# Kernel tuning notes

Measured on AMD Instinct MI355X. Metric: run time of the kernel, lower is better.

Reference implementation:

```python
import jax, jax.numpy as jnp
import numpy as np

D = 128      # feature dim
H = 8        # heads
DH = D // H  # dim per head
N = 100000   # nodes
E = 600000   # edges
BN_EPS = 1e-5


def _bn(x, g, b, m, v):
    # BatchNorm1d in eval mode (running stats)
    return (x - m) * jax.lax.rsqrt(v + BN_EPS) * g + b


def setup_inputs() -> dict:
    key = jax.random.key(0)
    ks = jax.random.split(key, 32)
    s = 1.0 / np.sqrt(D)
    inp = {
        "x": jax.random.normal(ks[0], (N, D), jnp.float32),
        "edge_index": jax.random.randint(ks[1], (2, E), 0, N, jnp.int64),
        # type embeddings (1 node type, 1 edge type)
        "nt_emb": jax.random.normal(ks[2], (1, D), jnp.float32),
        "et_emb": jax.random.normal(ks[3], (1, D), jnp.float32),
        # merge_node_edge_attr: Linear(2D,D) -> BN -> ReLU -> Linear(D,D)
        "mW1": jax.random.normal(ks[4], (2 * D, D), jnp.float32) * s,
        "mb1": jnp.zeros((D,), jnp.float32),
        "m_g": jnp.ones((D,), jnp.float32),
        "m_b": jnp.zeros((D,), jnp.float32),
        "m_m": jax.random.normal(ks[5], (D,), jnp.float32) * 0.1,
        "m_v": jax.random.uniform(ks[6], (D,), jnp.float32, 0.5, 1.5),
        "mW2": jax.random.normal(ks[7], (D, D), jnp.float32) * s,
        "mb2": jnp.zeros((D,), jnp.float32),
        # residual projection (no bias)
        "resW": jax.random.normal(ks[8], (D, D), jnp.float32) * s,
        # attention projections
        "qW": jax.random.normal(ks[9], (D, D), jnp.float32) * s,
        "qb": jnp.zeros((D,), jnp.float32),
        "kW": jax.random.normal(ks[10], (D, D), jnp.float32) * s,
        "kb": jnp.zeros((D,), jnp.float32),
        "vW": jax.random.normal(ks[11], (D, D), jnp.float32) * s,
        "vb": jnp.zeros((D,), jnp.float32),
        # output mlp: Linear -> BN -> LeakyReLU -> Linear
        "oW1": jax.random.normal(ks[12], (D, D), jnp.float32) * s,
        "ob1": jnp.zeros((D,), jnp.float32),
        "o_g": jnp.ones((D,), jnp.float32),
        "o_b": jnp.zeros((D,), jnp.float32),
        "o_m": jax.random.normal(ks[13], (D,), jnp.float32) * 0.1,
        "o_v": jax.random.uniform(ks[14], (D,), jnp.float32, 0.5, 1.5),
        "oW2": jax.random.normal(ks[15], (D, D), jnp.float32) * s,
        "ob2": jnp.zeros((D,), jnp.float32),
    }
    return inp


def reference(x, edge_index, nt_emb, et_emb, mW1, mb1, m_g, m_b, m_m, m_v, mW2, mb2,
              resW, qW, qb, kW, kb, vW, vb, oW1, ob1, o_g, o_b, o_m, o_v, oW2, ob2):
    src = edge_index[0]
    dst = edge_index[1]
    n_nodes = x.shape[0]
    e = edge_index.shape[1]

    # GraphNodeEdgeAttr: edge attrs are constant per edge type; with one node
    # type, edge_attr[0] == edge_attr[1] == merge(cat[node_emb, edge_emb]).
    merged = jnp.concatenate([nt_emb[0], et_emb[0]])          # [2D]
    h = jax.nn.relu(_bn(merged @ mW1 + mb1, m_g, m_b, m_m, m_v))
    ea = h @ mW2 + mb2                                        # [D], broadcasts per edge

    # edge_update: per-edge multi-head attention scores
    x_j = x[src]                                              # [E, D] source feats
    x_i = x[dst]                                              # [E, D] target feats
    q = ((x_j + ea) @ qW + qb).reshape(e, H, DH) / jnp.sqrt(jnp.float32(DH))
    k = ((x_i + ea) @ kW + kb).reshape(e, H, DH)
    msg = (x_j @ vW + vb).reshape(e, H, DH)
    scores = jnp.sum(q * k, axis=2)                           # [E, H]

    # segment softmax keyed by source node index
    smax = jax.ops.segment_max(scores, src, num_segments=n_nodes)
    ex = jnp.exp(scores - smax[src])
    ssum = jax.ops.segment_sum(ex, src, num_segments=n_nodes)
    alpha = ex / ssum[src]                                    # [E, H]

    # message + scatter-add aggregation to destination nodes
    weighted = (msg * alpha[:, :, None]).reshape(e, H * DH)   # [E, D]
    aggr = jax.ops.segment_sum(weighted, dst, num_segments=n_nodes)  # [N, D]

    res = x @ resW
    z = aggr + res
    out = jax.nn.leaky_relu(_bn(z @ oW1 + ob1, o_g, o_b, o_m, o_v)) @ oW2 + ob2
    return out
```

## Files before the change

### kernel.cpp

```cpp
#include <hip/hip_runtime.h>

#define BN_EPS 1e-5f
#define SCAN_CHUNK 1024
#define BM 128

typedef __attribute__((ext_vector_type(8))) short s16x8;
typedef __attribute__((ext_vector_type(4))) float f32x4;

__device__ __forceinline__ ushort f2bf_rne(float f)
{
    unsigned u = __builtin_bit_cast(unsigned, f);
    return (ushort)((u + 0x7fffu + ((u >> 16) & 1u)) >> 16);
}

__device__ __forceinline__ float bf2f(ushort u)
{
    return __builtin_bit_cast(float, (unsigned)u << 16);
}

__global__ __launch_bounds__(128) void k_ea(
    const float* __restrict__ nt, const float* __restrict__ et,
    const float* __restrict__ mW1, const float* __restrict__ mb1,
    const float* __restrict__ m_g, const float* __restrict__ m_b,
    const float* __restrict__ m_m, const float* __restrict__ m_v,
    const float* __restrict__ mW2, const float* __restrict__ mb2,
    const float* __restrict__ qW, const float* __restrict__ qb,
    const float* __restrict__ kW, const float* __restrict__ kb,
    float* __restrict__ eaq, float* __restrict__ eak)
{
    __shared__ float merged[256];
    __shared__ float h[128];
    __shared__ float sea[128];
    const int t = threadIdx.x;
    merged[t]       = nt[t];
    merged[128 + t] = et[t];
    __syncthreads();
    float acc = mb1[t];
    for (int i = 0; i < 256; ++i) acc = fmaf(merged[i], mW1[i * 128 + t], acc);
    acc = (acc - m_m[t]) * rsqrtf(m_v[t] + BN_EPS) * m_g[t] + m_b[t];
    h[t] = acc > 0.f ? acc : 0.f;
    __syncthreads();
    float acc2 = mb2[t];
    for (int k = 0; k < 128; ++k) acc2 = fmaf(h[k], mW2[k * 128 + t], acc2);
    sea[t] = acc2;
    __syncthreads();
    float aq = qb[t], ak = kb[t];
    for (int k = 0; k < 128; ++k) {
        const float e = sea[k];
        aq = fmaf(e, qW[k * 128 + t], aq);
        ak = fmaf(e, kW[k * 128 + t], ak);
    }
    eaq[t] = aq;
    eak[t] = ak;
}

__device__ __forceinline__ void split_store(float w, ushort* __restrict__ base,
                                            int j, int k)
{
    unsigned u = __builtin_bit_cast(unsigned, w);
    unsigned hi = (u + 0x7fffu + ((u >> 16) & 1u)) >> 16;
    float hif = __builtin_bit_cast(float, hi << 16);
    float res = w - hif;
    unsigned lo = __builtin_bit_cast(unsigned, res) >> 16;
    base[j * 128 + k]         = (ushort)hi;
    base[16384 + j * 128 + k] = (ushort)lo;
}

__global__ __launch_bounds__(128) void k_prep3(
    const float* __restrict__ W0, const float* __restrict__ W1,
    const float* __restrict__ W2, ushort* __restrict__ P)
{
    const int j = blockIdx.x;
    const int m = blockIdx.y;
    const int k = threadIdx.x;
    const float* W = (m == 0) ? W0 : (m == 1) ? W1 : W2;
    split_store(W[k * 128 + j], P + (size_t)m * 32768, j, k);
}

__global__ __launch_bounds__(128) void k_prep_out(
    const float* __restrict__ resW, const float* __restrict__ oW1,
    const float* __restrict__ oW2, ushort* __restrict__ P)
{
    __shared__ float col[128];
    const int j = blockIdx.x;
    const int m = blockIdx.y;
    const int k = threadIdx.x;
    float w;
    if (m == 0) {
        col[k] = oW1[k * 128 + j];
        __syncthreads();
        float acc = 0.f;
        for (int i = 0; i < 128; ++i) acc = fmaf(resW[k * 128 + i], col[i], acc);
        w = acc;
    } else {
        const float* W = (m == 1) ? oW1 : oW2;
        w = W[k * 128 + j];
    }
    split_store(w, P + (size_t)m * 32768, j, k);
}

template <int NT>
__device__ __forceinline__ void stage_w(const ushort* __restrict__ wpl,
                                        ushort* __restrict__ sw, int tid)
{
    const uint4* src = (const uint4*)wpl;
#pragma unroll
    for (int it = 0; it < 4096 / NT; ++it) {
        const int idx = it * NT + tid;
        const uint4 v = src[idx];
        const int plane = idx >> 11;
        const int rr = (idx >> 4) & 127;
        const int cb = (idx & 15) << 4;
        const int byteoff = ((rr * 256 + cb) ^ ((rr & 7) << 4));
        *(uint4*)((char*)sw + plane * 32768 + byteoff) = v;
    }
}

template <int NT>
__device__ __forceinline__ void stage_w1(const ushort* __restrict__ wpl,
                                         ushort* __restrict__ sw, int tid)
{
    const uint4* src = (const uint4*)wpl;
#pragma unroll
    for (int it = 0; it < 2048 / NT; ++it) {
        const int idx = it * NT + tid;
        const uint4 v = src[idx];
        const int rr = idx >> 4;
        const int cb = (idx & 15) << 4;
        const int byteoff = ((rr * 256 + cb) ^ ((rr & 7) << 4));
        *(uint4*)((char*)sw + byteoff) = v;
    }
}

__device__ __forceinline__ void split_row(const float* __restrict__ row, int g,
                                          s16x8* ah, s16x8* al)
{
#pragma unroll
    for (int ks = 0; ks < 4; ++ks) {
        const float* ap = row + ks * 32 + g * 8;
        const float4 a0 = *(const float4*)(ap);
        const float4 a1 = *(const float4*)(ap + 4);
        float av[8] = {a0.x, a0.y, a0.z, a0.w, a1.x, a1.y, a1.z, a1.w};
#pragma unroll
        for (int j = 0; j < 8; ++j) {
            const unsigned u = __builtin_bit_cast(unsigned, av[j]);
            ah[ks][j] = (short)(u >> 16);
            const float hif = __builtin_bit_cast(float, u & 0xffff0000u);
            const float res = av[j] - hif;
            al[ks][j] = (short)(__builtin_bit_cast(unsigned, res) >> 16);
        }
    }
}

template <int CT>
__device__ __forceinline__ void mm_core(const float* __restrict__ Arow,
                                        const ushort* __restrict__ sw,
                                        int g, int r16, int ct0, f32x4* acc)
{
#pragma unroll
    for (int ks = 0; ks < 4; ++ks) {
        const float* ap = Arow + ks * 32 + g * 8;
        const float4 a0 = *(const float4*)(ap);
        const float4 a1 = *(const float4*)(ap + 4);
        float av[8] = {a0.x, a0.y, a0.z, a0.w, a1.x, a1.y, a1.z, a1.w};
        s16x8 ahi, alo;
#pragma unroll
        for (int j = 0; j < 8; ++j) {
            const unsigned u = __builtin_bit_cast(unsigned, av[j]);
            ahi[j] = (short)(u >> 16);
            const float hif = __builtin_bit_cast(float, u & 0xffff0000u);
            const float res = av[j] - hif;
            alo[j] = (short)(__builtin_bit_cast(unsigned, res) >> 16);
        }
        const int koff = ks * 64 + g * 16;
#pragma unroll
        for (int ct = 0; ct < CT; ++ct) {
            const int row = (ct0 + ct) * 16 + r16;
            const int byteoff = ((row * 256 + koff) ^ ((row & 7) << 4));
            const s16x8 bhi = *(const s16x8*)((const char*)sw + byteoff);
            const s16x8 blo = *(const s16x8*)((const char*)sw + 32768 + byteoff);
            acc[ct] = __builtin_amdgcn_mfma_f32_16x16x32_bf16(ahi, bhi, acc[ct], 0, 0, 0);
            acc[ct] = __builtin_amdgcn_mfma_f32_16x16x32_bf16(ahi, blo, acc[ct], 0, 0, 0);
            acc[ct] = __builtin_amdgcn_mfma_f32_16x16x32_bf16(alo, bhi, acc[ct], 0, 0, 0);
        }
    }
}

template <int CT>
__device__ __forceinline__ void mm_pass2(const s16x8* ah, const s16x8* al,
                                         const ushort* __restrict__ sw,
                                         int g, int r16, int ct0, f32x4* acc)
{
#pragma unroll
    for (int ks = 0; ks < 4; ++ks) {
        const int koff = ks * 64 + g * 16;
#pragma unroll
        for (int ct = 0; ct < CT; ++ct) {
            const int row = (ct0 + ct) * 16 + r16;
            const int byteoff = ((row * 256 + koff) ^ ((row & 7) << 4));
            const s16x8 b = *(const s16x8*)((const char*)sw + byteoff);
            acc[ct] = __builtin_amdgcn_mfma_f32_16x16x32_bf16(ah[ks], b, acc[ct], 0, 0, 0);
            acc[ct] = __builtin_amdgcn_mfma_f32_16x16x32_bf16(al[ks], b, acc[ct], 0, 0, 0);
        }
    }
}

template <int CT>
__device__ __forceinline__ void mm_pass1(const s16x8* a,
                                         const ushort* __restrict__ sw,
                                         int g, int r16, int ct0, f32x4* acc)
{
#pragma unroll
    for (int ks = 0; ks < 4; ++ks) {
        const int koff = ks * 64 + g * 16;
#pragma unroll
        for (int ct = 0; ct < CT; ++ct) {
            const int row = (ct0 + ct) * 16 + r16;
            const int byteoff = ((row * 256 + koff) ^ ((row & 7) << 4));
            const s16x8 b = *(const s16x8*)((const char*)sw + byteoff);
            acc[ct] = __builtin_amdgcn_mfma_f32_16x16x32_bf16(a[ks], b, acc[ct], 0, 0, 0);
        }
    }
}

__global__ __launch_bounds__(1024, 8) void k_mm_qkv(
    const float* __restrict__ x, const ushort* __restrict__ planes,
    const float* __restrict__ eaq, const float* __restrict__ eak,
    const float* __restrict__ vb,
    float* __restrict__ Q, float* __restrict__ K, ushort* __restrict__ V16, int N)
{
    __shared__ ushort sw[2 * 128 * 128];
    const int tid = threadIdx.x;
    const int sel = blockIdx.y;
    stage_w<1024>(planes + (size_t)sel * 32768, sw, tid);
    __syncthreads();

    const int wave = tid >> 6, lane = tid & 63;
    const int g = lane >> 4, r16 = lane & 15;
    const int wr = wave & 7, wc = wave >> 3;
    const int ct0 = wc * 4;
    const int n0 = blockIdx.x * BM;
    const int arow = wr * 16 + r16;
    int nA = n0 + arow; if (nA >= N) nA = N - 1;

    f32x4 acc[4];
#pragma unroll
    for (int ct = 0; ct < 4; ++ct) acc[ct] = (f32x4){0.f, 0.f, 0.f, 0.f};
    mm_core<4>(x + (size_t)nA * 128, sw, g, r16, ct0, acc);

    if (sel == 2) {
        __syncthreads();
        ushort* vbuf = (ushort*)sw;
#pragma unroll
        for (int ct = 0; ct < 4; ++ct) {
            const int c = (ct0 + ct) * 16 + r16;
            const float bc = vb[c];
#pragma unroll
            for (int r = 0; r < 4; ++r) {
                const int nrel = wr * 16 + g * 4 + r;
                vbuf[nrel * 128 + c] = f2bf_rne(acc[ct][r] + bc);
            }
        }
        __syncthreads();
        const int row = tid >> 3;
        const int col = (tid & 7) * 16;
        if (n0 + row < N) {
            const uint4* src = (const uint4*)(vbuf + row * 128 + col);
            const uint4 v0 = src[0], v1 = src[1];
            uint4* dst = (uint4*)(V16 + (size_t)(n0 + row) * 128 + col);
            dst[0] = v0; dst[1] = v1;
        }
    } else {
        const float* bias = sel ? eak : eaq;
        float* O          = sel ? K   : Q;
        const float scale = sel ? 1.0f : 0.25f;
#pragma unroll
        for (int ct = 0; ct < 4; ++ct) {
            const int c = (ct0 + ct) * 16 + r16;
            const float bc = bias[c];
#pragma unroll
            for (int r = 0; r < 4; ++r) {
                const int n = n0 + wr * 16 + g * 4 + r;
                if (n < N) O[(size_t)n * 128 + c] = (acc[ct][r] + bc) * scale;
            }
        }
    }
}

__global__ __launch_bounds__(512, 4) void k_out3(
    const float* __restrict__ x, const ushort* __restrict__ Po,
    const float* __restrict__ aggr, const float* __restrict__ ob1,
    const float* __restrict__ o_m, const float* __restrict__ o_v,
    const float* __restrict__ o_g, const float* __restrict__ o_b,
    const float* __restrict__ ob2, float* __restrict__ out, int N)
{
    __shared__ ushort sw[128 * 128];
    __shared__ ushort tb[64 * 128];
    const int tid = threadIdx.x;
    const int wave = tid >> 6, lane = tid & 63;
    const int g = lane >> 4, r16 = lane & 15;
    const int wr = wave & 3, wc = wave >> 2;
    const int ct0 = wc * 4;
    const int n0 = blockIdx.x * 64;
    const int arow = wr * 16 + r16;
    int nA = n0 + arow; if (nA >= N) nA = N - 1;

    s16x8 ah[4], al[4];
    split_row(x + (size_t)nA * 128, g, ah, al);

    f32x4 acc[4];
#pragma unroll
    for (int ct = 0; ct < 4; ++ct) acc[ct] = (f32x4){0.f, 0.f, 0.f, 0.f};

    stage_w1<512>(Po, sw, tid); __syncthreads();
    mm_pass2<4>(ah, al, sw, g, r16, ct0, acc); __syncthreads();
    stage_w1<512>(Po + 16384, sw, tid); __syncthreads();
    mm_pass1<4>(ah, sw, g, r16, ct0, acc); __syncthreads();

    split_row(aggr + (size_t)nA * 128, g, ah, al);
    stage_w1<512>(Po + 32768, sw, tid); __syncthreads();
    mm_pass2<4>(ah, al, sw, g, r16, ct0, acc); __syncthreads();
    stage_w1<512>(Po + 49152, sw, tid); __syncthreads();
    mm_pass1<4>(ah, sw, g, r16, ct0, acc); __syncthreads();

#pragma unroll
    for (int ct = 0; ct < 4; ++ct) {
        const int c = (ct0 + ct) * 16 + r16;
        const float bc = ob1[c];
        const float rs = rsqrtf(o_v[c] + BN_EPS);
        const float mm = o_m[c], gg = o_g[c], bb = o_b[c];
#pragma unroll
        for (int r = 0; r < 4; ++r) {
            const int nrel = wr * 16 + g * 4 + r;
            float u = acc[ct][r] + bc;
            u = (u - mm) * rs * gg + bb;
            u = u > 0.f ? u : 0.01f * u;
            const int byteoff = ((nrel * 256 + c * 2) ^ ((nrel & 7) << 4));
            *(ushort*)((char*)tb + byteoff) = f2bf_rne(u);
        }
    }
    stage_w1<512>(Po + 65536, sw, tid);
    __syncthreads();

    s16x8 ta[4];
#pragma unroll
    for (int ks = 0; ks < 4; ++ks) {
        const int byteoff = ((arow * 256 + ks * 64 + g * 16) ^ ((arow & 7) << 4));
        ta[ks] = *(const s16x8*)((const char*)tb + byteoff);
    }
#pragma unroll
    for (int ct = 0; ct < 4; ++ct) acc[ct] = (f32x4){0.f, 0.f, 0.f, 0.f};
    mm_pass1<4>(ta, sw, g, r16, ct0, acc);
    __syncthreads();
    stage_w1<512>(Po + 81920, sw, tid); __syncthreads();
    mm_pass1<4>(ta, sw, g, r16, ct0, acc);

#pragma unroll
    for (int ct = 0; ct < 4; ++ct) {
        const int c = (ct0 + ct) * 16 + r16;
        const float bc = ob2[c];
#pragma unroll
        for (int r = 0; r < 4; ++r) {
            const int n = n0 + wr * 16 + g * 4 + r;
            if (n < N) out[(size_t)n * 128 + c] = acc[ct][r] + bc;
        }
    }
}

__global__ __launch_bounds__(256) void k_edge1csr(
    const int* __restrict__ esrc, const int* __restrict__ row_start,
    const int* __restrict__ deg, const float* __restrict__ Q,
    const float* __restrict__ K, float* __restrict__ exp_,
    float* __restrict__ ssum, int N)
{
    const int tid = threadIdx.x;
    const int n = blockIdx.x * 4 + (tid >> 6);
    if (n >= N) return;
    const int lane = tid & 63;
    const int sub = lane >> 5;
    const int l = lane & 31;
    const int h = l >> 2;
    const int c0 = l * 4;
    const int rs = row_start[n];
    const int dg = deg[n];
    const float4 kreg = *(const float4*)(K + (size_t)n * 128 + c0);
    for (int j = sub; j < dg; j += 2) {
        const int idx = rs + j;
        const int s = esrc[idx];
        const float4 q = *(const float4*)(Q + (size_t)s * 128 + c0);
        float p = q.x * kreg.x + q.y * kreg.y + q.z * kreg.z + q.w * kreg.w;
        p += __shfl_xor(p, 1, 64);
        p += __shfl_xor(p, 2, 64);
        if ((l & 3) == 0) {
            const float v = __expf(p);
            exp_[(size_t)idx * 8 + h] = v;
            unsafeAtomicAdd(&ssum[(size_t)s * 8 + h], v);
        }
    }
}

__global__ __launch_bounds__(256) void k_rsum(float* __restrict__ ssum, int M)
{
    const int i = blockIdx.x * 256 + threadIdx.x;
    if (i < M) ssum[i] = 1.0f / ssum[i];
}

__global__ __launch_bounds__(256) void k_hist(const int* __restrict__ ei,
                                              int* __restrict__ deg, int E)
{
    const int e = blockIdx.x * 256 + threadIdx.x;
    if (e < E) atomicAdd(&deg[ei[E + e]], 1);
}

__global__ __launch_bounds__(256) void k_scan_partial(const int* __restrict__ deg,
                                                      int* __restrict__ part, int N)
{
    __shared__ int sd[256];
    const int b = blockIdx.x, t = threadIdx.x;
    const int base = b * SCAN_CHUNK + t * 4;
    int s = 0;
#pragma unroll
    for (int i = 0; i < 4; ++i) { const int idx = base + i; if (idx < N) s += deg[idx]; }
    sd[t] = s; __syncthreads();
    for (int off = 128; off > 0; off >>= 1) {
        if (t < off) sd[t] += sd[t + off];
        __syncthreads();
    }
    if (t == 0) part[b] = sd[0];
}

__global__ __launch_bounds__(256) void k_scan_top(int* __restrict__ part, int nb)
{
    __shared__ int sd[256];
    const int t = threadIdx.x;
    const int orig = (t < nb) ? part[t] : 0;
    sd[t] = orig;
    __syncthreads();
    for (int off = 1; off < 256; off <<= 1) {
        const int v = (t >= off) ? sd[t - off] : 0;
        __syncthreads();
        sd[t] += v;
        __syncthreads();
    }
    if (t < nb) part[t] = sd[t] - orig;
}

__global__ __launch_bounds__(256) void k_scan_final(const int* __restrict__ deg,
                                                    const int* __restrict__ part,
                                                    int* __restrict__ row_start,
                                                    int* __restrict__ cursor, int N)
{
    __shared__ int ts[256];
    const int b = blockIdx.x, t = threadIdx.x;
    const int base = b * SCAN_CHUNK + t * 4;
    int v[4]; int s = 0;
#pragma unroll
    for (int i = 0; i < 4; ++i) { const int idx = base + i; v[i] = (idx < N) ? deg[idx] : 0; s += v[i]; }
    ts[t] = s; __syncthreads();
    for (int off = 1; off < 256; off <<= 1) {
        const int vv = (t >= off) ? ts[t - off] : 0;
        __syncthreads();
        ts[t] += vv;
        __syncthreads();
    }
    int run = part[b] + ((t > 0) ? ts[t - 1] : 0);
#pragma unroll
    for (int i = 0; i < 4; ++i) {
        const int idx = base + i;
        if (idx < N) { row_start[idx] = run; cursor[idx] = run; run += v[i]; }
    }
}

__global__ __launch_bounds__(256) void k_scatter(const int* __restrict__ ei,
                                                 int* __restrict__ cursor,
                                                 int* __restrict__ esrc, int E)
{
    const int e = blockIdx.x * 256 + threadIdx.x;
    if (e < E) {
        const int pos = atomicAdd(&cursor[ei[E + e]], 1);
        esrc[pos] = ei[e];
    }
}

__global__ __launch_bounds__(256) void k_aggr(
    const int* __restrict__ esrc, const int* __restrict__ row_start,
    const int* __restrict__ deg, const ushort* __restrict__ V16,
    const float* __restrict__ exp_, const float* __restrict__ rsum,
    float* __restrict__ aggr, int N)
{
    const int tid = threadIdx.x;
    const int n = blockIdx.x * 4 + (tid >> 6);
    if (n >= N) return;
    const int lane = tid & 63;
    const int sub = lane >> 5;
    const int l = lane & 31;
    const int h = l >> 2;
    const int c0 = l * 4;
    const int rs = row_start[n];
    const int dg = deg[n];
    float4 acc = make_float4(0.f, 0.f, 0.f, 0.f);
    for (int j = sub; j < dg; j += 2) {
        const int idx = rs + j;
        const int s = esrc[idx];
        const float a = exp_[(size_t)idx * 8 + h] * rsum[(size_t)s * 8 + h];
        const ushort4 vu = *(const ushort4*)(V16 + (size_t)s * 128 + c0);
        acc.x = fmaf(bf2f(vu.x), a, acc.x);
        acc.y = fmaf(bf2f(vu.y), a, acc.y);
        acc.z = fmaf(bf2f(vu.z), a, acc.z);
        acc.w = fmaf(bf2f(vu.w), a, acc.w);
    }
    acc.x += __shfl_xor(acc.x, 32, 64);
    acc.y += __shfl_xor(acc.y, 32, 64);
    acc.z += __shfl_xor(acc.z, 32, 64);
    acc.w += __shfl_xor(acc.w, 32, 64);
    if (sub == 0) *(float4*)(aggr + (size_t)n * 128 + c0) = acc;
}

extern "C" void kernel_launch(void* const* d_in, const int* in_sizes, int n_in,
                              void* d_out, int out_size, void* d_ws, size_t ws_size,
                              hipStream_t stream)
{
    const float* x    = (const float*)d_in[0];
    const int*   ei   = (const int*)d_in[1];
    const float* nt   = (const float*)d_in[2];
    const float* et   = (const float*)d_in[3];
    const float* mW1  = (const float*)d_in[4];
    const float* mb1  = (const float*)d_in[5];
    const float* m_g  = (const float*)d_in[6];
    const float* m_b  = (const float*)d_in[7];
    const float* m_m  = (const float*)d_in[8];
    const float* m_v  = (const float*)d_in[9];
    const float* mW2  = (const float*)d_in[10];
    const float* mb2  = (const float*)d_in[11];
    const float* resW = (const float*)d_in[12];
    const float* qW   = (const float*)d_in[13];
    const float* qb   = (const float*)d_in[14];
    const float* kW   = (const float*)d_in[15];
    const float* kb   = (const float*)d_in[16];
    const float* vW   = (const float*)d_in[17];
    const float* vb   = (const float*)d_in[18];
    const float* oW1  = (const float*)d_in[19];
    const float* ob1  = (const float*)d_in[20];
    const float* o_g  = (const float*)d_in[21];
    const float* o_b  = (const float*)d_in[22];
    const float* o_m  = (const float*)d_in[23];
    const float* o_v  = (const float*)d_in[24];
    const float* oW2  = (const float*)d_in[25];
    const float* ob2  = (const float*)d_in[26];
    float* out = (float*)d_out;

    const int N = in_sizes[0] / 128;
    const int E = in_sizes[1] / 2;

    float* ws   = (float*)d_ws;
    float* eaq  = ws;
    float* eak  = ws + 128;
    float* Q    = ws + 256;
    float* K    = Q + (size_t)N * 128;
    float* V    = K + (size_t)N * 128;
    float* exp_ = V + (size_t)N * 128;
    float* ssum = exp_ + (size_t)E * 8;
    int* deg       = (int*)(ssum + (size_t)N * 8);
    int* row_start = deg + N;
    int* cursor    = row_start + N;
    int* part      = cursor + N;
    int* esrc      = part + 256;
    float* aggr = Q;
    ushort* V16 = (ushort*)V;
    ushort* Pq = (ushort*)ssum;
    ushort* Po = (ushort*)exp_;

    const int nbm  = (N + BM - 1) / BM;
    const int nbo  = (N + 63) / 64;
    const int nbsc = (N + SCAN_CHUNK - 1) / SCAN_CHUNK;

    k_prep3<<<dim3(128, 3), 128, 0, stream>>>(qW, kW, vW, Pq);
    k_ea<<<1, 128, 0, stream>>>(nt, et, mW1, mb1, m_g, m_b, m_m, m_v, mW2, mb2,
                                qW, qb, kW, kb, eaq, eak);
    k_mm_qkv<<<dim3(nbm, 3), 1024, 0, stream>>>(x, Pq, eaq, eak, vb, Q, K, V16, N);

    hipMemsetAsync(ssum, 0, (size_t)N * 8 * sizeof(float), stream);
    hipMemsetAsync(deg, 0, (size_t)N * sizeof(int), stream);

    k_hist<<<(E + 255) / 256, 256, 0, stream>>>(ei, deg, E);
    k_scan_partial<<<nbsc, 256, 0, stream>>>(deg, part, N);
    k_scan_top<<<1, 256, 0, stream>>>(part, nbsc);
    k_scan_final<<<nbsc, 256, 0, stream>>>(deg, part, row_start, cursor, N);
    k_scatter<<<(E + 255) / 256, 256, 0, stream>>>(ei, cursor, esrc, E);

    k_edge1csr<<<(N + 3) / 4, 256, 0, stream>>>(esrc, row_start, deg, Q, K, exp_, ssum, N);
    k_rsum<<<(N * 8 + 255) / 256, 256, 0, stream>>>(ssum, N * 8);
    k_aggr<<<(N + 3) / 4, 256, 0, stream>>>(esrc, row_start, deg, V16, exp_, ssum, aggr, N);

    k_prep_out<<<dim3(128, 3), 128, 0, stream>>>(resW, oW1, oW2, Po);
    k_out3<<<nbo, 512, 0, stream>>>(x, Po, aggr, ob1, o_m, o_v, o_g, o_b, ob2, out, N);
}
```

Baseline: 485.1 us.

## Stage GEMM outputs through LDS for coalesced stores; widen per-lane edge vectors

The Q/K projection and output-MLP kernels now write their fp32 accumulators into a swizzled LDS buffer and then store whole rows to global memory with coalesced float4 writes, replacing scattered 4-byte stores. The edge-score and aggregation kernels now give each lane 8 channels, so 16 lanes cover a 128-wide row and each wave works on 4 edges at once instead of 2. The aim is better store coalescing and more edges in flight for the gather loads. The cost is extra barriers and LDS traffic in the GEMM epilogues, plus an extra shuffle stage in the aggregation reduction.

```diff
diff --git a/kernel.cpp b/kernel.cpp
--- a/kernel.cpp
+++ b/kernel.cpp
@@ -5,6 +5,7 @@
 #define BM 128
 
 typedef __attribute__((ext_vector_type(8))) short s16x8;
+typedef __attribute__((ext_vector_type(8))) ushort u16x8;
 typedef __attribute__((ext_vector_type(4))) float f32x4;
 
 __device__ __forceinline__ ushort f2bf_rne(float f)
@@ -247,9 +248,9 @@
 #pragma unroll
     for (int ct = 0; ct < 4; ++ct) acc[ct] = (f32x4){0.f, 0.f, 0.f, 0.f};
     mm_core<4>(x + (size_t)nA * 128, sw, g, r16, ct0, acc);
+    __syncthreads();
 
     if (sel == 2) {
-        __syncthreads();
         ushort* vbuf = (ushort*)sw;
 #pragma unroll
         for (int ct = 0; ct < 4; ++ct) {
@@ -274,15 +275,28 @@
         const float* bias = sel ? eak : eaq;
         float* O          = sel ? K   : Q;
         const float scale = sel ? 1.0f : 0.25f;
+        float* fbuf = (float*)sw;
 #pragma unroll
         for (int ct = 0; ct < 4; ++ct) {
             const int c = (ct0 + ct) * 16 + r16;
             const float bc = bias[c];
 #pragma unroll
             for (int r = 0; r < 4; ++r) {
-                const int n = n0 + wr * 16 + g * 4 + r;
-                if (n < N) O[(size_t)n * 128 + c] = (acc[ct][r] + bc) * scale;
+                const int nrel = wr * 16 + g * 4 + r;
+                const int byteoff = (nrel * 512 + c * 4) ^ ((nrel & 7) << 4);
+                *(float*)((char*)fbuf + byteoff) = (acc[ct][r] + bc) * scale;
             }
+        }
+        __syncthreads();
+        const float4* fb4 = (const float4*)fbuf;
+#pragma unroll
+        for (int it = 0; it < 4; ++it) {
+            const int idx4 = it * 1024 + tid;
+            const int row = idx4 >> 5;
+            const int n = n0 + row;
+            if (n < N)
+                *(float4*)(O + (size_t)n * 128 + (idx4 & 31) * 4) =
+                    fb4[row * 32 + ((idx4 & 31) ^ (row & 7))];
         }
     }
 }
@@ -354,16 +368,30 @@
     __syncthreads();
     stage_w1<512>(Po + 81920, sw, tid); __syncthreads();
     mm_pass1<4>(ta, sw, g, r16, ct0, acc);
-
+    __syncthreads();
+
+    float* fbuf = (float*)sw;
 #pragma unroll
     for (int ct = 0; ct < 4; ++ct) {
         const int c = (ct0 + ct) * 16 + r16;
         const float bc = ob2[c];
 #pragma unroll
         for (int r = 0; r < 4; ++r) {
-            const int n = n0 + wr * 16 + g * 4 + r;
-            if (n < N) out[(size_t)n * 128 + c] = acc[ct][r] + bc;
-        }
+            const int nrel = wr * 16 + g * 4 + r;
+            const int byteoff = (nrel * 512 + c * 4) ^ ((nrel & 7) << 4);
+            *(float*)((char*)fbuf + byteoff) = acc[ct][r] + bc;
+        }
+    }
+    __syncthreads();
+    const float4* fb4 = (const float4*)fbuf;
+#pragma unroll
+    for (int it = 0; it < 4; ++it) {
+        const int idx4 = it * 512 + tid;
+        const int row = idx4 >> 5;
+        const int n = n0 + row;
+        if (n < N)
+            *(float4*)(out + (size_t)n * 128 + (idx4 & 31) * 4) =
+                fb4[row * 32 + ((idx4 & 31) ^ (row & 7))];
     }
 }
 
@@ -377,21 +405,23 @@
     const int n = blockIdx.x * 4 + (tid >> 6);
     if (n >= N) return;
     const int lane = tid & 63;
-    const int sub = lane >> 5;
-    const int l = lane & 31;
-    const int h = l >> 2;
-    const int c0 = l * 4;
+    const int sub = lane >> 4;
+    const int l = lane & 15;
+    const int h = l >> 1;
+    const int c0 = l * 8;
     const int rs = row_start[n];
     const int dg = deg[n];
-    const float4 kreg = *(const float4*)(K + (size_t)n * 128 + c0);
-    for (int j = sub; j < dg; j += 2) {
+    const float4 k0 = *(const float4*)(K + (size_t)n * 128 + c0);
+    const float4 k1 = *(const float4*)(K + (size_t)n * 128 + c0 + 4);
+    for (int j = sub; j < dg; j += 4) {
         const int idx = rs + j;
         const int s = esrc[idx];
-        const float4 q = *(const float4*)(Q + (size_t)s * 128 + c0);
-        float p = q.x * kreg.x + q.y * kreg.y + q.z * kreg.z + q.w * kreg.w;
+        const float4 q0 = *(const float4*)(Q + (size_t)s * 128 + c0);
+        const float4 q1 = *(const float4*)(Q + (size_t)s * 128 + c0 + 4);
+        float p = q0.x * k0.x + q0.y * k0.y + q0.z * k0.z + q0.w * k0.w
+                + q1.x * k1.x + q1.y * k1.y + q1.z * k1.z + q1.w * k1.w;
         p += __shfl_xor(p, 1, 64);
-        p += __shfl_xor(p, 2, 64);
-        if ((l & 3) == 0) {
+        if ((l & 1) == 0) {
             const float v = __expf(p);
             exp_[(size_t)idx * 8 + h] = v;
             unsafeAtomicAdd(&ssum[(size_t)s * 8 + h], v);
@@ -492,28 +522,42 @@
     const int n = blockIdx.x * 4 + (tid >> 6);
     if (n >= N) return;
     const int lane = tid & 63;
-    const int sub = lane >> 5;
-    const int l = lane & 31;
-    const int h = l >> 2;
-    const int c0 = l * 4;
+    const int sub = lane >> 4;
+    const int l = lane & 15;
+    const int h = l >> 1;
+    const int c0 = l * 8;
     const int rs = row_start[n];
     const int dg = deg[n];
-    float4 acc = make_float4(0.f, 0.f, 0.f, 0.f);
-    for (int j = sub; j < dg; j += 2) {
+    float a0 = 0.f, a1 = 0.f, a2 = 0.f, a3 = 0.f;
+    float a4 = 0.f, a5 = 0.f, a6 = 0.f, a7 = 0.f;
+    for (int j = sub; j < dg; j += 4) {
         const int idx = rs + j;
         const int s = esrc[idx];
         const float a = exp_[(size_t)idx * 8 + h] * rsum[(size_t)s * 8 + h];
-        const ushort4 vu = *(const ushort4*)(V16 + (size_t)s * 128 + c0);
-        acc.x = fmaf(bf2f(vu.x), a, acc.x);
-        acc.y = fmaf(bf2f(vu.y), a, acc.y);
-        acc.z = fmaf(bf2f(vu.z), a, acc.z);
-        acc.w = fmaf(bf2f(vu.w), a, acc.w);
-    }
-    acc.x += __shfl_xor(acc.x, 32, 64);
-    acc.y += __shfl_xor(acc.y, 32, 64);
-    acc.z += __shfl_xor(acc.z, 32, 64);
-    acc.w += __shfl_xor(acc.w, 32, 64);
-    if (sub == 0) *(float4*)(aggr + (size_t)n * 128 + c0) = acc;
+        const u16x8 vu = *(const u16x8*)(V16 + (size_t)s * 128 + c0);
+        a0 = fmaf(bf2f(vu[0]), a, a0);
+        a1 = fmaf(bf2f(vu[1]), a, a1);
+        a2 = fmaf(bf2f(vu[2]), a, a2);
+        a3 = fmaf(bf2f(vu[3]), a, a3);
+        a4 = fmaf(bf2f(vu[4]), a, a4);
+        a5 = fmaf(bf2f(vu[5]), a, a5);
+        a6 = fmaf(bf2f(vu[6]), a, a6);
+        a7 = fmaf(bf2f(vu[7]), a, a7);
+    }
+    a0 += __shfl_xor(a0, 16, 64); a0 += __shfl_xor(a0, 32, 64);
+    a1 += __shfl_xor(a1, 16, 64); a1 += __shfl_xor(a1, 32, 64);
+    a2 += __shfl_xor(a2, 16, 64); a2 += __shfl_xor(a2, 32, 64);
+    a3 += __shfl_xor(a3, 16, 64); a3 += __shfl_xor(a3, 32, 64);
+    a4 += __shfl_xor(a4, 16, 64); a4 += __shfl_xor(a4, 32, 64);
+    a5 += __shfl_xor(a5, 16, 64); a5 += __shfl_xor(a5, 32, 64);
+    a6 += __shfl_xor(a6, 16, 64); a6 += __shfl_xor(a6, 32, 64);
+    a7 += __shfl_xor(a7, 16, 64); a7 += __shfl_xor(a7, 32, 64);
+    if (sub == 0) {
+        float4 o0 = make_float4(a0, a1, a2, a3);
+        float4 o1 = make_float4(a4, a5, a6, a7);
+        *(float4*)(aggr + (size_t)n * 128 + c0)     = o0;
+        *(float4*)(aggr + (size_t)n * 128 + c0 + 4) = o1;
+    }
 }
 
 extern "C" void kernel_launch(void* const* d_in, const int* in_sizes, int n_in,
```

Measured after the change: 450.3 us. 7.2% less time.
